# Kernel optimization log

Hardware: AMD Instinct MI355X
Metric: run time of the kernel (lower is better)

The kernel has to match this reference:

```python
import jax, jax.numpy as jnp
import numpy as np

NUM_TOKENS = 1024  # codebook size (n_embed)
CODE_DIM = 256     # embedding_dim
BETA = 0.25


def setup_inputs() -> dict:
    key = jax.random.key(0)
    k1, k2 = jax.random.split(key)
    z = jax.random.normal(k1, (64, 512, CODE_DIM), dtype=jnp.float32)
    weight = jax.random.normal(k2, (NUM_TOKENS, CODE_DIM), dtype=jnp.float32)
    return {"z": z, "weight": weight}


def reference(z, weight):
    # z: [B, T, D]; weight: [K, D]
    z_flat = z.reshape(-1, CODE_DIM)                       # [N, D]
    # squared euclidean distances: ||z||^2 + ||w||^2 - 2 z.w
    d = (jnp.sum(z_flat ** 2, axis=1, keepdims=True)
         + jnp.sum(weight ** 2, axis=1)
         - 2.0 * jnp.matmul(z_flat, weight.T))             # [N, K]
    min_encoding_indices = jnp.argmin(d, axis=1)           # [N]
    z_q = weight[min_encoding_indices].reshape(z.shape)    # gather

    # perplexity from mean one-hot usage (avoid materializing one-hot via bincount)
    counts = jnp.bincount(min_encoding_indices, length=NUM_TOKENS)
    e_mean = counts.astype(z.dtype) / z_flat.shape[0]
    perplexity = jnp.exp(-jnp.sum(e_mean * jnp.log(e_mean + 1e-10)))

    # commitment loss (codebook is EMA-updated, so z_q is detached)
    loss = BETA * jnp.mean((jax.lax.stop_gradient(z_q) - z) ** 2)
    # straight-through estimator
    z_q_st = z + jax.lax.stop_gradient(z_q - z)
    return (loss, z_q_st, min_encoding_indices, perplexity)
```

## Files before the change

kernel.cpp:

```cpp
#include <hip/hip_runtime.h>

#define N_TOKENS 32768
#define K_CODES  1024
#define DIM      256
#define BETA     0.25f

typedef unsigned long long u64;
typedef _Float16 half8 __attribute__((ext_vector_type(8)));
typedef float floatx4 __attribute__((ext_vector_type(4)));

__global__ void init_kernel(const float* __restrict__ w, float* __restrict__ wn,
                            int* __restrict__ counts, u64* __restrict__ keys,
                            _Float16* __restrict__ whiG, _Float16* __restrict__ wloG) {
    int k = blockIdx.x;
    int lane = threadIdx.x;
    float4 v = *(const float4*)(w + (size_t)k * DIM + lane * 4);
    float vals[4] = {v.x, v.y, v.z, v.w};
    float s = 0.f;
    #pragma unroll
    for (int e = 0; e < 4; e++) {
        s += vals[e] * vals[e];
        _Float16 h = (_Float16)vals[e];
        whiG[k * DIM + lane * 4 + e] = h;
        wloG[k * DIM + lane * 4 + e] = (_Float16)(vals[e] - (float)h);
    }
    #pragma unroll
    for (int off = 32; off; off >>= 1) s += __shfl_down(s, off);
    if (lane == 0) { wn[k] = s; counts[k] = 0; }
    if (lane < 32) keys[k * 32 + lane] = ~0ull;
}

__global__ __launch_bounds__(256, 4) void argmin_kernel(
    const float* __restrict__ z, const _Float16* __restrict__ whiG,
    const _Float16* __restrict__ wloG, const float* __restrict__ wn,
    u64* __restrict__ keys)
{
    constexpr int ZS = 40;
    __shared__ _Float16 zhi[128 * ZS], zlo[128 * ZS];
    __shared__ _Float16 whi[128 * ZS], wlo[128 * ZS];

    const int tid  = threadIdx.x;
    const int lane = tid & 63;
    const int wid  = tid >> 6;
    const int wm   = wid >> 1;
    const int wq   = wid & 1;
    const int t_   = blockIdx.x & 255;
    const int q8   = blockIdx.x >> 8;
    const int tok0  = t_ * 128;
    const int kbase = q8 * 128;

    float wnr[4];
    #pragma unroll
    for (int j = 0; j < 4; j++)
        wnr[j] = wn[kbase + wq * 64 + j * 16 + (lane & 15)];

    floatx4 acc[4][4];
    #pragma unroll
    for (int i = 0; i < 4; i++)
        #pragma unroll
        for (int j = 0; j < 4; j++)
            acc[i][j] = (floatx4){0.f, 0.f, 0.f, 0.f};

    const int r0 = tid >> 2;
    const int g0 = tid & 3;

    for (int dt = 0; dt < 8; ++dt) {
        const int d0 = dt * 32;
        __syncthreads();

        #pragma unroll
        for (int s = 0; s < 2; s++) {
            int t = r0 + s * 64;
            const float* p = z + (size_t)(tok0 + t) * DIM + d0 + g0 * 8;
            float4 a = *(const float4*)p;
            float4 b = *(const float4*)(p + 4);
            float vals[8] = {a.x, a.y, a.z, a.w, b.x, b.y, b.z, b.w};
            half8 hv, lv;
            #pragma unroll
            for (int e = 0; e < 8; e++) {
                _Float16 h = (_Float16)vals[e];
                hv[e] = h;
                lv[e] = (_Float16)(vals[e] - (float)h);
            }
            *(half8*)&zhi[t * ZS + g0 * 8] = hv;
            *(half8*)&zlo[t * ZS + g0 * 8] = lv;
        }
        #pragma unroll
        for (int s = 0; s < 2; s++) {
            int t = r0 + s * 64;
            size_t goff = (size_t)(kbase + t) * DIM + d0 + g0 * 8;
            *(half8*)&whi[t * ZS + g0 * 8] = *(const half8*)&whiG[goff];
            *(half8*)&wlo[t * ZS + g0 * 8] = *(const half8*)&wloG[goff];
        }
        __syncthreads();

        const int koff = (lane >> 4) * 8;
        half8 ah[4], al[4];
        #pragma unroll
        for (int i = 0; i < 4; i++) {
            int off = (wm * 64 + i * 16 + (lane & 15)) * ZS + koff;
            ah[i] = *(const half8*)&zhi[off];
            al[i] = *(const half8*)&zlo[off];
        }
        __builtin_amdgcn_s_setprio(1);
        #pragma unroll
        for (int j = 0; j < 4; j++) {
            int off = (wq * 64 + j * 16 + (lane & 15)) * ZS + koff;
            half8 bh = *(const half8*)&whi[off];
            half8 bl = *(const half8*)&wlo[off];
            #pragma unroll
            for (int i = 0; i < 4; i++) {
                acc[i][j] = __builtin_amdgcn_mfma_f32_16x16x32_f16(ah[i], bh, acc[i][j], 0, 0, 0);
                acc[i][j] = __builtin_amdgcn_mfma_f32_16x16x32_f16(ah[i], bl, acc[i][j], 0, 0, 0);
                acc[i][j] = __builtin_amdgcn_mfma_f32_16x16x32_f16(al[i], bh, acc[i][j], 0, 0, 0);
            }
        }
        __builtin_amdgcn_s_setprio(0);
    }

    #pragma unroll
    for (int i = 0; i < 4; i++) {
        #pragma unroll
        for (int r = 0; r < 4; r++) {
            float bv = 3.4e38f; int bi = 0;
            #pragma unroll
            for (int j = 0; j < 4; j++) {
                int cl = wq * 64 + j * 16 + (lane & 15);
                float dist = wnr[j] - 2.0f * acc[i][j][r];
                if (dist < bv) { bv = dist; bi = kbase + cl; }
            }
            unsigned uu = __float_as_uint(bv);
            unsigned ss = (uu & 0x80000000u) ? ~uu : (uu | 0x80000000u);
            u64 key = ((u64)ss << 32) | (unsigned)bi;
            #pragma unroll
            for (int m = 1; m < 16; m <<= 1) {
                u64 o = __shfl_xor(key, m);
                if (o < key) key = o;
            }
            if ((lane & 15) == 0) {
                int token = tok0 + wm * 64 + i * 16 + (lane >> 4) * 4 + r;
                atomicMin(&keys[token], key);
            }
        }
    }
}

__global__ void gather_loss_kernel(const float* __restrict__ z,
                                   const float* __restrict__ w,
                                   const u64* __restrict__ keys,
                                   float* __restrict__ zq_out,
                                   float* __restrict__ idxf,
                                   int* __restrict__ counts,
                                   float* __restrict__ partials)
{
    __shared__ float red[4];
    int tid = threadIdx.x;
    int lane = tid & 63;
    int wid = blockIdx.x * 4 + (tid >> 6);
    float s = 0.0f;
    #pragma unroll
    for (int it = 0; it < 4; it++) {
        int tok = wid + it * 8192;
        u64 key = 0;
        if (lane == 0) key = keys[tok];
        key = __shfl(key, 0);
        int k = (int)(key & (u64)(K_CODES - 1));
        float4 wv = *(const float4*)(w + (size_t)k * DIM + lane * 4);
        float4 zv = *(const float4*)(z + (size_t)tok * DIM + lane * 4);
        *(float4*)(zq_out + (size_t)tok * DIM + lane * 4) = wv;
        float dx = wv.x - zv.x, dy = wv.y - zv.y, dz = wv.z - zv.z, dw = wv.w - zv.w;
        s += dx * dx + dy * dy + dz * dz + dw * dw;
        if (lane == 0) {
            idxf[tok] = (float)k;
            atomicAdd(&counts[k], 1);
        }
    }
    #pragma unroll
    for (int off = 32; off; off >>= 1) s += __shfl_down(s, off);
    if (lane == 0) red[tid >> 6] = s;
    __syncthreads();
    if (tid == 0)
        partials[blockIdx.x] = red[0] + red[1] + red[2] + red[3];
}

__global__ void finalize_kernel(const int* __restrict__ counts,
                                const float* __restrict__ partials,
                                float* __restrict__ loss_out,
                                float* __restrict__ ppl_out)
{
    __shared__ float redE[16], redL[16];
    int tid = threadIdx.x;
    float e = (float)counts[tid] * (1.0f / (float)N_TOKENS);
    float t = -e * logf(e + 1e-10f);
    float p = partials[tid] + partials[tid + 1024];
    #pragma unroll
    for (int off = 32; off; off >>= 1) {
        t += __shfl_down(t, off);
        p += __shfl_down(p, off);
    }
    if ((tid & 63) == 0) { redE[tid >> 6] = t; redL[tid >> 6] = p; }
    __syncthreads();
    if (tid == 0) {
        float se = 0.0f, sl = 0.0f;
        #pragma unroll
        for (int i = 0; i < 16; i++) { se += redE[i]; sl += redL[i]; }
        *ppl_out = expf(se);
        *loss_out = BETA * sl / (float)((size_t)N_TOKENS * DIM);
    }
}

extern "C" void kernel_launch(void* const* d_in, const int* in_sizes, int n_in,
                              void* d_out, int out_size, void* d_ws, size_t ws_size,
                              hipStream_t stream) {
    const float* z = (const float*)d_in[0];
    const float* w = (const float*)d_in[1];
    float* out = (float*)d_out;

    float* loss_out = out;
    float* zq_out   = out + 1;
    float* idxf     = out + 1 + (size_t)N_TOKENS * DIM;
    float* ppl_out  = out + (out_size - 1);

    float* wn       = (float*)d_ws;
    int*   counts   = (int*)d_ws + 1024;
    float* partials = (float*)d_ws + 2048;
    u64*   keys     = (u64*)((char*)d_ws + 16384);
    _Float16* whiG  = (_Float16*)((char*)d_ws + 16384 + (size_t)N_TOKENS * 8);
    _Float16* wloG  = whiG + (size_t)K_CODES * DIM;

    init_kernel<<<K_CODES, 64, 0, stream>>>(w, wn, counts, keys, whiG, wloG);
    argmin_kernel<<<8 * 256, 256, 0, stream>>>(z, whiG, wloG, wn, keys);
    gather_loss_kernel<<<2048, 256, 0, stream>>>(z, w, keys, zq_out, idxf, counts, partials);
    finalize_kernel<<<1, 1024, 0, stream>>>(counts, partials, loss_out, ppl_out);
}
```

Measured before the change: 170.4 us.

## Pre-swizzle codebook tiles and double-buffer them via direct global-to-LDS loads

The init kernel now writes the split fp16 codebook in a tiled, XOR-swizzled layout that matches the LDS tile. The argmin kernel streams each tile straight into a double-buffered LDS region with global_load_lds, prefetching the next d-slice while MFMAs run on the current one. This removes the register round-trip for weight loads and overlaps weight fetch with compute. The cost is more LDS per block, so launch bounds drop from 4 to 3 blocks per CU, which lowers occupancy.

```diff
diff --git a/kernel.cpp b/kernel.cpp
--- a/kernel.cpp
+++ b/kernel.cpp
@@ -7,37 +7,56 @@
 
 typedef unsigned long long u64;
 typedef _Float16 half8 __attribute__((ext_vector_type(8)));
+typedef _Float16 half4 __attribute__((ext_vector_type(4)));
 typedef float floatx4 __attribute__((ext_vector_type(4)));
+
+__device__ __forceinline__ void glds16(const void* g, void* l) {
+    __builtin_amdgcn_global_load_lds(
+        (const __attribute__((address_space(1))) void*)g,
+        (__attribute__((address_space(3))) void*)l, 16, 0, 0);
+}
 
 __global__ void init_kernel(const float* __restrict__ w, float* __restrict__ wn,
                             int* __restrict__ counts, u64* __restrict__ keys,
-                            _Float16* __restrict__ whiG, _Float16* __restrict__ wloG) {
+                            _Float16* __restrict__ wG) {
     int k = blockIdx.x;
     int lane = threadIdx.x;
     float4 v = *(const float4*)(w + (size_t)k * DIM + lane * 4);
     float vals[4] = {v.x, v.y, v.z, v.w};
+
+    int q8  = k >> 7;
+    int row = k & 127;
+    int d0  = lane * 4;
+    int dt  = d0 >> 5;
+    int c0  = d0 & 31;
+    int bofs = (2 * c0) ^ ((row & 3) << 4);
+    char* dst = (char*)wG + (size_t)(q8 * 8 + dt) * 16384 + row * 64 + bofs;
+
+    half4 hv, lv;
     float s = 0.f;
     #pragma unroll
     for (int e = 0; e < 4; e++) {
         s += vals[e] * vals[e];
         _Float16 h = (_Float16)vals[e];
-        whiG[k * DIM + lane * 4 + e] = h;
-        wloG[k * DIM + lane * 4 + e] = (_Float16)(vals[e] - (float)h);
-    }
+        hv[e] = h;
+        lv[e] = (_Float16)(vals[e] - (float)h);
+    }
+    *(half4*)dst = hv;
+    *(half4*)(dst + 8192) = lv;
+
     #pragma unroll
     for (int off = 32; off; off >>= 1) s += __shfl_down(s, off);
     if (lane == 0) { wn[k] = s; counts[k] = 0; }
     if (lane < 32) keys[k * 32 + lane] = ~0ull;
 }
 
-__global__ __launch_bounds__(256, 4) void argmin_kernel(
-    const float* __restrict__ z, const _Float16* __restrict__ whiG,
-    const _Float16* __restrict__ wloG, const float* __restrict__ wn,
-    u64* __restrict__ keys)
+__global__ __launch_bounds__(256, 3) void argmin_kernel(
+    const float* __restrict__ z, const _Float16* __restrict__ wG,
+    const float* __restrict__ wn, u64* __restrict__ keys)
 {
     constexpr int ZS = 40;
     __shared__ _Float16 zhi[128 * ZS], zlo[128 * ZS];
-    __shared__ _Float16 whi[128 * ZS], wlo[128 * ZS];
+    __shared__ __attribute__((aligned(16))) char wbuf[2][16384];
 
     const int tid  = threadIdx.x;
     const int lane = tid & 63;
@@ -63,8 +82,18 @@
 
     const int r0 = tid >> 2;
     const int g0 = tid & 3;
+    const int kg = lane >> 4;
+
+    const int rb = (wq * 64 + (lane & 15)) * 64 + ((kg * 16) ^ ((lane & 3) << 4));
+
+    const char* wGq = (const char*)wG + (size_t)q8 * (8 * 16384) + wid * 4096 + lane * 16;
+
+    #pragma unroll
+    for (int c = 0; c < 4; c++)
+        glds16(wGq + c * 1024, &wbuf[0][wid * 4096 + c * 1024]);
 
     for (int dt = 0; dt < 8; ++dt) {
+        const int cur = dt & 1;
         const int d0 = dt * 32;
         __syncthreads();
 
@@ -85,16 +114,17 @@
             *(half8*)&zhi[t * ZS + g0 * 8] = hv;
             *(half8*)&zlo[t * ZS + g0 * 8] = lv;
         }
-        #pragma unroll
-        for (int s = 0; s < 2; s++) {
-            int t = r0 + s * 64;
-            size_t goff = (size_t)(kbase + t) * DIM + d0 + g0 * 8;
-            *(half8*)&whi[t * ZS + g0 * 8] = *(const half8*)&whiG[goff];
-            *(half8*)&wlo[t * ZS + g0 * 8] = *(const half8*)&wloG[goff];
-        }
         __syncthreads();
 
-        const int koff = (lane >> 4) * 8;
+        if (dt < 7) {
+            const char* src = wGq + (dt + 1) * 16384;
+            char* ldst = &wbuf[cur ^ 1][wid * 4096];
+            #pragma unroll
+            for (int c = 0; c < 4; c++)
+                glds16(src + c * 1024, ldst + c * 1024);
+        }
+
+        const int koff = kg * 8;
         half8 ah[4], al[4];
         #pragma unroll
         for (int i = 0; i < 4; i++) {
@@ -105,9 +135,9 @@
         __builtin_amdgcn_s_setprio(1);
         #pragma unroll
         for (int j = 0; j < 4; j++) {
-            int off = (wq * 64 + j * 16 + (lane & 15)) * ZS + koff;
-            half8 bh = *(const half8*)&whi[off];
-            half8 bl = *(const half8*)&wlo[off];
+            const char* pb = &wbuf[cur][rb + j * 1024];
+            half8 bh = *(const half8*)pb;
+            half8 bl = *(const half8*)(pb + 8192);
             #pragma unroll
             for (int i = 0; i < 4; i++) {
                 acc[i][j] = __builtin_amdgcn_mfma_f32_16x16x32_f16(ah[i], bh, acc[i][j], 0, 0, 0);
@@ -225,11 +255,10 @@
     int*   counts   = (int*)d_ws + 1024;
     float* partials = (float*)d_ws + 2048;
     u64*   keys     = (u64*)((char*)d_ws + 16384);
-    _Float16* whiG  = (_Float16*)((char*)d_ws + 16384 + (size_t)N_TOKENS * 8);
-    _Float16* wloG  = whiG + (size_t)K_CODES * DIM;
-
-    init_kernel<<<K_CODES, 64, 0, stream>>>(w, wn, counts, keys, whiG, wloG);
-    argmin_kernel<<<8 * 256, 256, 0, stream>>>(z, whiG, wloG, wn, keys);
+    _Float16* wG    = (_Float16*)((char*)d_ws + 16384 + (size_t)N_TOKENS * 8);
+
+    init_kernel<<<K_CODES, 64, 0, stream>>>(w, wn, counts, keys, wG);
+    argmin_kernel<<<8 * 256, 256, 0, stream>>>(z, wG, wn, keys);
     gather_loss_kernel<<<2048, 256, 0, stream>>>(z, w, keys, zq_out, idxf, counts, partials);
     finalize_kernel<<<1, 1024, 0, stream>>>(counts, partials, loss_out, ppl_out);
 }
```

Result: no change. 168.0 us (-1.4%).
